# Kernel tuning notes

Measured on AMD Instinct MI355X. Metric: run time of the kernel, lower is better.

Reference implementation:

```python
import jax, jax.numpy as jnp
import numpy as np

C = 1024
N_HEADS = 16
HEAD_DIM = C // N_HEADS
D_FF = 4 * C
EPS = 1e-5


def setup_inputs() -> dict:
    key = jax.random.key(0)
    ks = jax.random.split(key, 6)
    B, T = 4, 2048
    x = jax.random.normal(ks[0], (B, T, C), dtype=jnp.float32)
    w_qkv = jax.random.normal(ks[1], (C, 3 * C), dtype=jnp.float32) * (C ** -0.5)
    w_proj = jax.random.normal(ks[2], (C, C), dtype=jnp.float32) * (C ** -0.5)
    w1 = jax.random.normal(ks[3], (C, D_FF), dtype=jnp.float32) * (C ** -0.5)
    b1 = jnp.zeros((D_FF,), dtype=jnp.float32)
    w2 = jax.random.normal(ks[4], (D_FF, C), dtype=jnp.float32) * (D_FF ** -0.5)
    b2 = jnp.zeros((C,), dtype=jnp.float32)
    ln1_g = jnp.ones((C,), dtype=jnp.float32)
    ln1_b = jnp.zeros((C,), dtype=jnp.float32)
    ln2_g = jnp.ones((C,), dtype=jnp.float32)
    ln2_b = jnp.zeros((C,), dtype=jnp.float32)
    return {"x": x, "ln1_g": ln1_g, "ln1_b": ln1_b, "ln2_g": ln2_g,
            "ln2_b": ln2_b, "w_qkv": w_qkv, "w_proj": w_proj,
            "w1": w1, "b1": b1, "w2": w2, "b2": b2}


def _layernorm(x, g, b):
    mu = jnp.mean(x, axis=-1, keepdims=True)
    var = jnp.mean(jnp.square(x - mu), axis=-1, keepdims=True)
    return (x - mu) * jax.lax.rsqrt(var + EPS) * g + b


def _attention(x, w_qkv, w_proj):
    B, T, Cdim = x.shape
    qkv = x @ w_qkv                                   # [B,T,3C]
    q, k, v = jnp.split(qkv, 3, axis=-1)
    # [B,T,C] -> [B,H,T,D]
    def heads(t):
        return t.reshape(B, T, N_HEADS, HEAD_DIM).transpose(0, 2, 1, 3)
    q, k, v = heads(q), heads(k), heads(v)
    scale = HEAD_DIM ** -0.5
    scores = jnp.einsum('bhqd,bhkd->bhqk', q, k) * scale  # [B,H,T,T]
    attn = jax.nn.softmax(scores, axis=-1)
    out = jnp.einsum('bhqk,bhkd->bhqd', attn, v)          # [B,H,T,D]
    out = out.transpose(0, 2, 1, 3).reshape(B, T, Cdim)
    return out @ w_proj


def reference(x, ln1_g, ln1_b, ln2_g, ln2_b, w_qkv, w_proj, w1, b1, w2, b2):
    x = x + _attention(_layernorm(x, ln1_g, ln1_b), w_qkv, w_proj)
    h = _layernorm(x, ln2_g, ln2_b)
    # exact (erf) GELU matches torch.nn.GELU default
    h = jax.nn.gelu(h @ w1 + b1, approximate=False) @ w2 + b2
    return x + h
```

## Files before the change

kernel.cpp:

```cpp
#include <hip/hip_runtime.h>
#include <hip/hip_bf16.h>
#include <math.h>

typedef __attribute__((ext_vector_type(8))) short bf16x8;
typedef __attribute__((ext_vector_type(4))) float f32x4;
typedef unsigned short ushort_t;

__device__ __forceinline__ ushort_t f2bf(float f) {
    union { float f; unsigned u; } v; v.f = f;
    unsigned r = v.u + 0x7FFF + ((v.u >> 16) & 1);
    return (ushort_t)(r >> 16);
}

__device__ __forceinline__ unsigned pack2bf(float a, float b) {
    union { float f; unsigned u; } x, y; x.f = a; y.f = b;
    return __builtin_amdgcn_perm(y.u + 0x8000u, x.u + 0x8000u, 0x07060302u);
}

__device__ __forceinline__ void gl2lds(const void* g, void* l) {
    __builtin_amdgcn_global_load_lds(
        (const __attribute__((address_space(1))) void*)g,
        (__attribute__((address_space(3))) void*)l, 16, 0, 0);
}

__device__ __forceinline__ float fast_gelu(float tt) {
    float t2 = tt * tt;
    float arg = tt * fmaf(0.07135481283f, t2, 1.595769122f);
    float e = __builtin_amdgcn_exp2f(arg * -1.442695041f);
    return tt * __builtin_amdgcn_rcpf(1.0f + e);
}

__global__ __launch_bounds__(256)
void tcast_kernel(const float* __restrict__ in, ushort_t* __restrict__ out,
                  int R, int Cc, int scale_n, float scale) {
    __shared__ float tile[32][33];
    int bc = blockIdx.x * 32, br = blockIdx.y * 32;
    int tx = threadIdx.x, ty = threadIdx.y;
    #pragma unroll
    for (int i = 0; i < 32; i += 8)
        tile[ty + i][tx] = in[(size_t)(br + ty + i) * Cc + bc + tx];
    __syncthreads();
    #pragma unroll
    for (int i = 0; i < 32; i += 8) {
        int n = bc + ty + i;
        float v = tile[tx][ty + i];
        if (n < scale_n) v *= scale;
        out[(size_t)n * R + br + tx] = f2bf(v);
    }
}

__global__ __launch_bounds__(256)
void vtrans_kernel(const ushort_t* __restrict__ qkvb, ushort_t* __restrict__ vT) {
    __shared__ ushort_t tile[32][33];
    int bc = blockIdx.x * 32, br = blockIdx.y * 32;
    int tx = threadIdx.x, ty = threadIdx.y;
    #pragma unroll
    for (int i = 0; i < 32; i += 8)
        tile[ty + i][tx] = qkvb[(size_t)(br + ty + i) * 3072 + 2048 + bc + tx];
    __syncthreads();
    #pragma unroll
    for (int i = 0; i < 32; i += 8) {
        int c2 = bc + ty + i;
        int h = c2 >> 6, d = c2 & 63;
        int r2 = br + tx;
        int bb = r2 >> 11, t = r2 & 2047;
        vT[(((size_t)bb * 16 + h) * 64 + d) * 2048 + t] = tile[tx][ty + i];
    }
}

__global__ __launch_bounds__(256)
void ln_kernel(const float* __restrict__ x, const float* __restrict__ g,
               const float* __restrict__ b, ushort_t* __restrict__ out) {
    const int row = blockIdx.x;
    const int t = threadIdx.x;
    const float4 xv = ((const float4*)(x + (size_t)row * 1024))[t];
    float s  = xv.x + xv.y + xv.z + xv.w;
    float ss = xv.x*xv.x + xv.y*xv.y + xv.z*xv.z + xv.w*xv.w;
    #pragma unroll
    for (int off = 32; off > 0; off >>= 1) {
        s  += __shfl_xor(s, off);
        ss += __shfl_xor(ss, off);
    }
    __shared__ float red[8];
    int wave = t >> 6, lane = t & 63;
    if (lane == 0) { red[wave] = s; red[4 + wave] = ss; }
    __syncthreads();
    s  = red[0] + red[1] + red[2] + red[3];
    ss = red[4] + red[5] + red[6] + red[7];
    float mu  = s * (1.0f / 1024.0f);
    float var = ss * (1.0f / 1024.0f) - mu * mu;
    float rstd = rsqrtf(var + 1e-5f);
    float4 gv = ((const float4*)g)[t];
    float4 bv = ((const float4*)b)[t];
    ushort4 o;
    o.x = f2bf((xv.x - mu) * rstd * gv.x + bv.x);
    o.y = f2bf((xv.y - mu) * rstd * gv.y + bv.y);
    o.z = f2bf((xv.z - mu) * rstd * gv.z + bv.z);
    o.w = f2bf((xv.w - mu) * rstd * gv.w + bv.w);
    ((ushort4*)(out + (size_t)row * 1024))[t] = o;
}

template<int MODE, int K, int N>
__global__ __launch_bounds__(256)
void gemm_bt(const ushort_t* __restrict__ A, const ushort_t* __restrict__ Bt,
             void* __restrict__ Cout, const float* __restrict__ bias,
             const float* __restrict__ res) {
    constexpr int BK = 64;
    __shared__ __align__(16) ushort_t As[128 * 64];
    __shared__ __align__(16) ushort_t Bs[128 * 64];
    const int tid = threadIdx.x;
    const int wave = tid >> 6, lane = tid & 63;
    const int quad = lane >> 4, l16 = lane & 15;
    const int m0 = blockIdx.y * 128, n0 = blockIdx.x * 128;
    const int wm = (wave >> 1) * 64, wn = (wave & 1) * 64;

    const int r0 = tid >> 3, pc = tid & 7;
    const int lc = pc ^ (r0 & 7);
    const ushort_t* aSrc = A  + (size_t)(m0 + r0) * K + lc * 8;
    const ushort_t* bSrc = Bt + (size_t)(n0 + r0) * K + lc * 8;
    char* aDst = (char*)As + wave * 1024;
    char* bDst = (char*)Bs + wave * 1024;
    const int swz = l16 & 7;

    f32x4 acc[4][4] = {};

    for (int k0 = 0; k0 < K; k0 += BK) {
        __syncthreads();
        #pragma unroll
        for (int c = 0; c < 4; ++c) {
            gl2lds(aSrc + (size_t)c * 32 * K + k0, aDst + c * 4096);
            gl2lds(bSrc + (size_t)c * 32 * K + k0, bDst + c * 4096);
        }
        __syncthreads();
        #pragma unroll
        for (int ks = 0; ks < 2; ++ks) {
            const int cko = ((ks * 4 + quad) ^ swz) * 8;
            bf16x8 af[4], bfr[4];
            #pragma unroll
            for (int i = 0; i < 4; ++i)
                af[i] = *(const bf16x8*)(&As[(wm + i * 16 + l16) * 64 + cko]);
            #pragma unroll
            for (int j = 0; j < 4; ++j)
                bfr[j] = *(const bf16x8*)(&Bs[(wn + j * 16 + l16) * 64 + cko]);
            #pragma unroll
            for (int i = 0; i < 4; ++i)
                #pragma unroll
                for (int j = 0; j < 4; ++j)
                    acc[i][j] = __builtin_amdgcn_mfma_f32_16x16x32_bf16(
                        af[i], bfr[j], acc[i][j], 0, 0, 0);
        }
    }

    float bj[4];
    if constexpr (MODE == 2 || MODE == 3) {
        #pragma unroll
        for (int j = 0; j < 4; ++j) bj[j] = bias[n0 + wn + j * 16 + l16];
    }
    #pragma unroll
    for (int i = 0; i < 4; ++i) {
        #pragma unroll
        for (int j = 0; j < 4; ++j) {
            #pragma unroll
            for (int r = 0; r < 4; ++r) {
                int m = m0 + wm + i * 16 + quad * 4 + r;
                int n = n0 + wn + j * 16 + l16;
                size_t idx = (size_t)m * N + n;
                float v = acc[i][j][r];
                if constexpr (MODE == 0) {
                    ((ushort_t*)Cout)[idx] = f2bf(v);
                } else if constexpr (MODE == 1) {
                    ((float*)Cout)[idx] = v + res[idx];
                } else if constexpr (MODE == 2) {
                    ((ushort_t*)Cout)[idx] = f2bf(fast_gelu(v + bj[j]));
                } else {
                    ((float*)Cout)[idx] = v + bj[j] + res[idx];
                }
            }
        }
    }
}

__global__ __launch_bounds__(256)
void attn_kernel(const ushort_t* __restrict__ qkv, const ushort_t* __restrict__ vT,
                 ushort_t* __restrict__ out) {
    constexpr int T = 2048, C3 = 3072, BQ = 128, LDP = 72;
    __shared__ __align__(16) ushort_t Ks[64 * 64];
    __shared__ __align__(16) ushort_t Vs[64 * 64];
    __shared__ __align__(16) ushort_t Ps[BQ * LDP];
    const int bh = blockIdx.y, b = bh >> 4, h = bh & 15;
    const int qt = blockIdx.x;
    const int tid = threadIdx.x, wave = tid >> 6, lane = tid & 63;
    const int quad = lane >> 4, l16 = lane & 15;
    const int swz = l16 & 7;

    bf16x8 qf[2][2];
    {
        const ushort_t* Qg = qkv + ((size_t)b * T + qt * BQ + wave * 32) * C3 + h * 64;
        #pragma unroll
        for (int i = 0; i < 2; ++i)
            #pragma unroll
            for (int ks = 0; ks < 2; ++ks)
                qf[i][ks] = *(const bf16x8*)(Qg + (size_t)(i * 16 + l16) * C3 + ks * 32 + quad * 8);
    }
    const int r0 = tid >> 3, pc = tid & 7;
    const int lc = pc ^ (r0 & 7);
    const ushort_t* Kg = qkv + (size_t)b * T * C3 + 1024 + h * 64 + (size_t)r0 * C3 + lc * 8;
    const ushort_t* Vg = vT + (size_t)bh * 64 * T + (size_t)r0 * T + lc * 8;

    f32x4 o_acc[2][4] = {};
    float l_part[2] = {0.0f, 0.0f};
    const int prow = (wave * 32 + l16) * LDP;

    for (int kt = 0; kt < T / 64; ++kt) {
        __syncthreads();
        #pragma unroll
        for (int c = 0; c < 2; ++c) {
            gl2lds(Kg + ((size_t)kt * 64 + c * 32) * C3, (char*)Ks + c * 4096 + wave * 1024);
            gl2lds(Vg + (size_t)c * 32 * T + kt * 64,    (char*)Vs + c * 4096 + wave * 1024);
        }
        __syncthreads();

        f32x4 s[2][4] = {};
        #pragma unroll
        for (int ks = 0; ks < 2; ++ks) {
            const int cko = ((ks * 4 + quad) ^ swz) * 8;
            bf16x8 kf[4];
            #pragma unroll
            for (int j = 0; j < 4; ++j)
                kf[j] = *(const bf16x8*)(&Ks[(j * 16 + l16) * 64 + cko]);
            #pragma unroll
            for (int i = 0; i < 2; ++i)
                #pragma unroll
                for (int j = 0; j < 4; ++j)
                    s[i][j] = __builtin_amdgcn_mfma_f32_16x16x32_bf16(
                        kf[j], qf[i][ks], s[i][j], 0, 0, 0);
        }

        #pragma unroll
        for (int i = 0; i < 2; ++i) {
            #pragma unroll
            for (int j = 0; j < 4; ++j) {
                float p0 = __builtin_amdgcn_exp2f(s[i][j][0]);
                float p1 = __builtin_amdgcn_exp2f(s[i][j][1]);
                float p2 = __builtin_amdgcn_exp2f(s[i][j][2]);
                float p3 = __builtin_amdgcn_exp2f(s[i][j][3]);
                l_part[i] += (p0 + p1) + (p2 + p3);
                uint2 pk;
                pk.x = pack2bf(p0, p1);
                pk.y = pack2bf(p2, p3);
                *(uint2*)(&Ps[prow + i * 16 * LDP + j * 16 + quad * 4]) = pk;
            }
        }

        #pragma unroll
        for (int ks2 = 0; ks2 < 2; ++ks2) {
            const int ko = ks2 * 32 + quad * 8;
            const int cko = ((ks2 * 4 + quad) ^ swz) * 8;
            bf16x8 pf[2], vf[4];
            #pragma unroll
            for (int i = 0; i < 2; ++i)
                pf[i] = *(const bf16x8*)(&Ps[prow + i * 16 * LDP + ko]);
            #pragma unroll
            for (int j = 0; j < 4; ++j)
                vf[j] = *(const bf16x8*)(&Vs[(j * 16 + l16) * 64 + cko]);
            #pragma unroll
            for (int i = 0; i < 2; ++i)
                #pragma unroll
                for (int j = 0; j < 4; ++j)
                    o_acc[i][j] = __builtin_amdgcn_mfma_f32_16x16x32_bf16(
                        pf[i], vf[j], o_acc[i][j], 0, 0, 0);
        }
    }

    #pragma unroll
    for (int i = 0; i < 2; ++i) {
        float lt = l_part[i];
        lt += __shfl_xor(lt, 16);
        lt += __shfl_xor(lt, 32);
        #pragma unroll
        for (int r = 0; r < 4; ++r) {
            float lv = __shfl(lt, quad * 4 + r);
            float inv = 1.0f / lv;
            int row = qt * BQ + wave * 32 + i * 16 + quad * 4 + r;
            size_t orow = ((size_t)b * T + row) * 1024 + h * 64;
            #pragma unroll
            for (int j = 0; j < 4; ++j)
                out[orow + j * 16 + l16] = f2bf(o_acc[i][j][r] * inv);
        }
    }
}

extern "C" void kernel_launch(void* const* d_in, const int* in_sizes, int n_in,
                              void* d_out, int out_size, void* d_ws, size_t ws_size,
                              hipStream_t stream) {
    const float* x     = (const float*)d_in[0];
    const float* ln1g  = (const float*)d_in[1];
    const float* ln1b  = (const float*)d_in[2];
    const float* ln2g  = (const float*)d_in[3];
    const float* ln2b  = (const float*)d_in[4];
    const float* wqkv  = (const float*)d_in[5];
    const float* wproj = (const float*)d_in[6];
    const float* w1    = (const float*)d_in[7];
    const float* b1    = (const float*)d_in[8];
    const float* w2    = (const float*)d_in[9];
    const float* b2    = (const float*)d_in[10];
    float* out = (float*)d_out;

    const size_t MT = 8192;
    ushort_t* wqkvT  = (ushort_t*)d_ws;
    ushort_t* wprojT = wqkvT  + (size_t)3072 * 1024;
    ushort_t* w1T    = wprojT + (size_t)1024 * 1024;
    ushort_t* w2T    = w1T    + (size_t)4096 * 1024;
    ushort_t* xn     = w2T    + (size_t)1024 * 4096;
    ushort_t* qkvb   = xn     + MT * 1024;
    ushort_t* attnb  = qkvb   + MT * 3072;
    float*    x2     = (float*)(attnb + MT * 1024);
    ushort_t* xn2    = (ushort_t*)(x2 + MT * 1024);
    ushort_t* h1     = xn;
    ushort_t* vT     = (ushort_t*)x2;

    dim3 blk256(256);
    dim3 tblk(32, 8);
    const float qscale = 0.125f * 1.4426950408889634f;

    tcast_kernel<<<dim3(96, 32),  tblk, 0, stream>>>(wqkv,  wqkvT,  1024, 3072, 1024, qscale);
    tcast_kernel<<<dim3(32, 32),  tblk, 0, stream>>>(wproj, wprojT, 1024, 1024, 0, 1.0f);
    tcast_kernel<<<dim3(128, 32), tblk, 0, stream>>>(w1,    w1T,    1024, 4096, 0, 1.0f);
    tcast_kernel<<<dim3(32, 128), tblk, 0, stream>>>(w2,    w2T,    4096, 1024, 0, 1.0f);

    ln_kernel<<<dim3(8192), blk256, 0, stream>>>(x, ln1g, ln1b, xn);
    gemm_bt<0, 1024, 3072><<<dim3(24, 64), blk256, 0, stream>>>(xn, wqkvT, qkvb, nullptr, nullptr);
    vtrans_kernel<<<dim3(32, 256), tblk, 0, stream>>>(qkvb, vT);
    attn_kernel<<<dim3(16, 64), blk256, 0, stream>>>(qkvb, vT, attnb);
    gemm_bt<1, 1024, 1024><<<dim3(8, 64), blk256, 0, stream>>>(attnb, wprojT, x2, nullptr, x);
    ln_kernel<<<dim3(8192), blk256, 0, stream>>>(x2, ln2g, ln2b, xn2);
    gemm_bt<2, 1024, 4096><<<dim3(32, 64), blk256, 0, stream>>>(xn2, w1T, h1, b1, nullptr);
    gemm_bt<3, 4096, 1024><<<dim3(8, 64), blk256, 0, stream>>>(h1, w2T, out, b2, x2);
}
```

Baseline: 501.5 us.

## Fuse V transpose into QKV GEMM, double-buffer attention K/V, merge weight casts

```diff
diff --git a/kernel.cpp b/kernel.cpp
--- a/kernel.cpp
+++ b/kernel.cpp
@@ -31,10 +31,19 @@
 }
 
 __global__ __launch_bounds__(256)
-void tcast_kernel(const float* __restrict__ in, ushort_t* __restrict__ out,
-                  int R, int Cc, int scale_n, float scale) {
+void tcast_all(const float* __restrict__ wqkv, const float* __restrict__ wproj,
+               const float* __restrict__ w1, const float* __restrict__ w2,
+               ushort_t* __restrict__ wqkvT, ushort_t* __restrict__ wprojT,
+               ushort_t* __restrict__ w1T, ushort_t* __restrict__ w2T,
+               float qscale) {
     __shared__ float tile[32][33];
-    int bc = blockIdx.x * 32, br = blockIdx.y * 32;
+    int id = blockIdx.x;
+    const float* in; ushort_t* out; int R, Cc, gx, scale_n;
+    if (id < 3072)      { in = wqkv;  out = wqkvT;  R = 1024; Cc = 3072; gx = 96;  scale_n = 1024; }
+    else if (id < 4096) { id -= 3072; in = wproj; out = wprojT; R = 1024; Cc = 1024; gx = 32; scale_n = 0; }
+    else if (id < 8192) { id -= 4096; in = w1;    out = w1T;    R = 1024; Cc = 4096; gx = 128; scale_n = 0; }
+    else                { id -= 8192; in = w2;    out = w2T;    R = 4096; Cc = 1024; gx = 32; scale_n = 0; }
+    int bc = (id % gx) * 32, br = (id / gx) * 32;
     int tx = threadIdx.x, ty = threadIdx.y;
     #pragma unroll
     for (int i = 0; i < 32; i += 8)
@@ -44,27 +53,8 @@
     for (int i = 0; i < 32; i += 8) {
         int n = bc + ty + i;
         float v = tile[tx][ty + i];
-        if (n < scale_n) v *= scale;
+        if (n < scale_n) v *= qscale;
         out[(size_t)n * R + br + tx] = f2bf(v);
-    }
-}
-
-__global__ __launch_bounds__(256)
-void vtrans_kernel(const ushort_t* __restrict__ qkvb, ushort_t* __restrict__ vT) {
-    __shared__ ushort_t tile[32][33];
-    int bc = blockIdx.x * 32, br = blockIdx.y * 32;
-    int tx = threadIdx.x, ty = threadIdx.y;
-    #pragma unroll
-    for (int i = 0; i < 32; i += 8)
-        tile[ty + i][tx] = qkvb[(size_t)(br + ty + i) * 3072 + 2048 + bc + tx];
-    __syncthreads();
-    #pragma unroll
-    for (int i = 0; i < 32; i += 8) {
-        int c2 = bc + ty + i;
-        int h = c2 >> 6, d = c2 & 63;
-        int r2 = br + tx;
-        int bb = r2 >> 11, t = r2 & 2047;
-        vT[(((size_t)bb * 16 + h) * 64 + d) * 2048 + t] = tile[tx][ty + i];
     }
 }
 
@@ -104,7 +94,7 @@
 __global__ __launch_bounds__(256)
 void gemm_bt(const ushort_t* __restrict__ A, const ushort_t* __restrict__ Bt,
              void* __restrict__ Cout, const float* __restrict__ bias,
-             const float* __restrict__ res) {
+             const float* __restrict__ res, ushort_t* __restrict__ vTout) {
     constexpr int BK = 64;
     __shared__ __align__(16) ushort_t As[128 * 64];
     __shared__ __align__(16) ushort_t Bs[128 * 64];
@@ -151,6 +141,25 @@
         }
     }
 
+    if constexpr (MODE == 0) {
+        if (vTout && n0 >= 2048) {
+            #pragma unroll
+            for (int i = 0; i < 4; ++i) {
+                int m = m0 + wm + i * 16 + quad * 4;
+                int bb = m >> 11, t = m & 2047;
+                #pragma unroll
+                for (int j = 0; j < 4; ++j) {
+                    int nn = n0 - 2048 + wn + j * 16 + l16;
+                    int h = nn >> 6, d = nn & 63;
+                    uint2 pk;
+                    pk.x = pack2bf(acc[i][j][0], acc[i][j][1]);
+                    pk.y = pack2bf(acc[i][j][2], acc[i][j][3]);
+                    *(uint2*)(vTout + ((size_t)(bb * 16 + h) * 64 + d) * 2048 + t) = pk;
+                }
+            }
+            return;
+        }
+    }
     float bj[4];
     if constexpr (MODE == 2 || MODE == 3) {
         #pragma unroll
@@ -183,10 +192,10 @@
 __global__ __launch_bounds__(256)
 void attn_kernel(const ushort_t* __restrict__ qkv, const ushort_t* __restrict__ vT,
                  ushort_t* __restrict__ out) {
-    constexpr int T = 2048, C3 = 3072, BQ = 128, LDP = 72;
-    __shared__ __align__(16) ushort_t Ks[64 * 64];
-    __shared__ __align__(16) ushort_t Vs[64 * 64];
-    __shared__ __align__(16) ushort_t Ps[BQ * LDP];
+    constexpr int T = 2048, C3 = 3072, BQ = 128;
+    __shared__ __align__(16) ushort_t Ks[2][64 * 64];
+    __shared__ __align__(16) ushort_t Vs[2][64 * 64];
+    __shared__ __align__(16) ushort_t Ps[BQ * 64];
     const int bh = blockIdx.y, b = bh >> 4, h = bh & 15;
     const int qt = blockIdx.x;
     const int tid = threadIdx.x, wave = tid >> 6, lane = tid & 63;
@@ -204,21 +213,34 @@
     }
     const int r0 = tid >> 3, pc = tid & 7;
     const int lc = pc ^ (r0 & 7);
-    const ushort_t* Kg = qkv + (size_t)b * T * C3 + 1024 + h * 64 + (size_t)r0 * C3 + lc * 8;
-    const ushort_t* Vg = vT + (size_t)bh * 64 * T + (size_t)r0 * T + lc * 8;
+    const ushort_t* KgB = qkv + (size_t)b * T * C3 + 1024 + h * 64 + (size_t)r0 * C3 + lc * 8;
+    const ushort_t* VgB = vT + (size_t)bh * 64 * T + (size_t)r0 * T + lc * 8;
+    char* kDst0 = (char*)&Ks[0][0] + wave * 1024;
+    char* vDst0 = (char*)&Vs[0][0] + wave * 1024;
 
     f32x4 o_acc[2][4] = {};
     float l_part[2] = {0.0f, 0.0f};
-    const int prow = (wave * 32 + l16) * LDP;
+    const int prow = (wave * 32 + l16) * 64;
+
+    #pragma unroll
+    for (int c = 0; c < 2; ++c) {
+        gl2lds(KgB + (size_t)c * 32 * C3, kDst0 + c * 4096);
+        gl2lds(VgB + (size_t)c * 32 * T,  vDst0 + c * 4096);
+    }
 
     for (int kt = 0; kt < T / 64; ++kt) {
+        const int cur = kt & 1;
         __syncthreads();
-        #pragma unroll
-        for (int c = 0; c < 2; ++c) {
-            gl2lds(Kg + ((size_t)kt * 64 + c * 32) * C3, (char*)Ks + c * 4096 + wave * 1024);
-            gl2lds(Vg + (size_t)c * 32 * T + kt * 64,    (char*)Vs + c * 4096 + wave * 1024);
-        }
-        __syncthreads();
+        if (kt + 1 < T / 64) {
+            const int nb = (cur ^ 1) * 8192;
+            #pragma unroll
+            for (int c = 0; c < 2; ++c) {
+                gl2lds(KgB + ((size_t)(kt + 1) * 64 + c * 32) * C3, kDst0 + nb + c * 4096);
+                gl2lds(VgB + (size_t)c * 32 * T + (kt + 1) * 64,    vDst0 + nb + c * 4096);
+            }
+        }
+        const ushort_t* Kc = &Ks[cur][0];
+        const ushort_t* Vc = &Vs[cur][0];
 
         f32x4 s[2][4] = {};
         #pragma unroll
@@ -227,7 +249,7 @@
             bf16x8 kf[4];
             #pragma unroll
             for (int j = 0; j < 4; ++j)
-                kf[j] = *(const bf16x8*)(&Ks[(j * 16 + l16) * 64 + cko]);
+                kf[j] = *(const bf16x8*)(&Kc[(j * 16 + l16) * 64 + cko]);
             #pragma unroll
             for (int i = 0; i < 2; ++i)
                 #pragma unroll
@@ -248,21 +270,21 @@
                 uint2 pk;
                 pk.x = pack2bf(p0, p1);
                 pk.y = pack2bf(p2, p3);
-                *(uint2*)(&Ps[prow + i * 16 * LDP + j * 16 + quad * 4]) = pk;
+                const int c2 = (j * 2 + (quad >> 1)) ^ swz;
+                *(uint2*)(&Ps[prow + i * 16 * 64 + c2 * 8 + (quad & 1) * 4]) = pk;
             }
         }
 
         #pragma unroll
         for (int ks2 = 0; ks2 < 2; ++ks2) {
-            const int ko = ks2 * 32 + quad * 8;
             const int cko = ((ks2 * 4 + quad) ^ swz) * 8;
             bf16x8 pf[2], vf[4];
             #pragma unroll
             for (int i = 0; i < 2; ++i)
-                pf[i] = *(const bf16x8*)(&Ps[prow + i * 16 * LDP + ko]);
+                pf[i] = *(const bf16x8*)(&Ps[prow + i * 16 * 64 + cko]);
             #pragma unroll
             for (int j = 0; j < 4; ++j)
-                vf[j] = *(const bf16x8*)(&Vs[(j * 16 + l16) * 64 + cko]);
+                vf[j] = *(const bf16x8*)(&Vc[(j * 16 + l16) * 64 + cko]);
             #pragma unroll
             for (int i = 0; i < 2; ++i)
                 #pragma unroll
@@ -323,17 +345,14 @@
     dim3 tblk(32, 8);
     const float qscale = 0.125f * 1.4426950408889634f;
 
-    tcast_kernel<<<dim3(96, 32),  tblk, 0, stream>>>(wqkv,  wqkvT,  1024, 3072, 1024, qscale);
-    tcast_kernel<<<dim3(32, 32),  tblk, 0, stream>>>(wproj, wprojT, 1024, 1024, 0, 1.0f);
-    tcast_kernel<<<dim3(128, 32), tblk, 0, stream>>>(w1,    w1T,    1024, 4096, 0, 1.0f);
-    tcast_kernel<<<dim3(32, 128), tblk, 0, stream>>>(w2,    w2T,    4096, 1024, 0, 1.0f);
+    tcast_all<<<dim3(12288), tblk, 0, stream>>>(wqkv, wproj, w1, w2,
+                                                wqkvT, wprojT, w1T, w2T, qscale);
 
     ln_kernel<<<dim3(8192), blk256, 0, stream>>>(x, ln1g, ln1b, xn);
-    gemm_bt<0, 1024, 3072><<<dim3(24, 64), blk256, 0, stream>>>(xn, wqkvT, qkvb, nullptr, nullptr);
-    vtrans_kernel<<<dim3(32, 256), tblk, 0, stream>>>(qkvb, vT);
+    gemm_bt<0, 1024, 3072><<<dim3(24, 64), blk256, 0, stream>>>(xn, wqkvT, qkvb, nullptr, nullptr, vT);
     attn_kernel<<<dim3(16, 64), blk256, 0, stream>>>(qkvb, vT, attnb);
-    gemm_bt<1, 1024, 1024><<<dim3(8, 64), blk256, 0, stream>>>(attnb, wprojT, x2, nullptr, x);
+    gemm_bt<1, 1024, 1024><<<dim3(8, 64), blk256, 0, stream>>>(attnb, wprojT, x2, nullptr, x, nullptr);
     ln_kernel<<<dim3(8192), blk256, 0, stream>>>(x2, ln2g, ln2b, xn2);
-    gemm_bt<2, 1024, 4096><<<dim3(32, 64), blk256, 0, stream>>>(xn2, w1T, h1, b1, nullptr);
-    gemm_bt<3, 4096, 1024><<<dim3(8, 64), blk256, 0, stream>>>(h1, w2T, out, b2, x2);
-}
+    gemm_bt<2, 1024, 4096><<<dim3(32, 64), blk256, 0, stream>>>(xn2, w1T, h1, b1, nullptr, nullptr);
+    gemm_bt<3, 4096, 1024><<<dim3(8, 64), blk256, 0, stream>>>(h1, w2T, out, b2, x2, nullptr);
+}
```

Result: no change. 505.6 us (+0.8%).
